# Optimization experiments

Measured on AMD Instinct MI355X. Metric: run time of the kernel, lower is better.

The kernel has to match this reference:

```python
import jax, jax.numpy as jnp
import numpy as np

B, D_IN, U, E = 8192, 1024, 1024, 16

def setup_inputs() -> dict:
    key = jax.random.key(0)
    k1, k2, k3, k4 = jax.random.split(key, 4)
    inputs = jax.random.normal(k1, (B, D_IN), dtype=jnp.float32)
    # type_prob: probability over entity types per example, [B, E, 1]
    tp = jax.random.uniform(k2, (B, E, 1), dtype=jnp.float32)
    type_prob = tp / jnp.sum(tp, axis=1, keepdims=True)
    # Stacked per-entity Dense params: W [E, D_IN, U], b [E, U]
    scale = 1.0 / np.sqrt(D_IN)
    W = jax.random.normal(k3, (E, D_IN, U), dtype=jnp.float32) * scale
    b = jax.random.normal(k4, (E, U), dtype=jnp.float32) * 0.01
    return {"inputs": inputs, "type_prob": type_prob, "W": W, "b": b}

def reference(inputs, type_prob, W, b):
    # Per-entity Dense, batched as one einsum: [B, E, U]
    logits = jnp.einsum('bd,edu->beu', inputs, W) + b
    probs = jax.nn.softmax(logits, axis=-1)  # softmax over wp_units, per entity
    # transpose to [B, U, E], matmul with type_prob [B, E, 1], reduce_sum last axis
    # == weighted combine over entities: [B, U]
    result = jnp.einsum('beu,be->bu', probs, type_prob[..., 0])
    return result
```

## Files before the change

### kernel.cpp

```cpp
#include <hip/hip_runtime.h>
#include <hip/hip_bf16.h>
#include <hip/hip_fp16.h>
#include <stdint.h>

typedef _Float16 f16;
typedef _Float16 f16x4 __attribute__((ext_vector_type(4)));
typedef _Float16 f16x8 __attribute__((ext_vector_type(8)));
typedef float f32x4 __attribute__((ext_vector_type(4)));

#define NB 8192
#define ND 1024
#define NU 1024
#define NE 16

__global__ __launch_bounds__(256) void k_prep(const float* __restrict__ W,
                                              f16* __restrict__ WT,
                                              const float* __restrict__ X,
                                              f16* __restrict__ Xh) {
  const int bid = blockIdx.x;
  const int t = threadIdx.x;
  if (bid < 4096) {
    __shared__ f16 tile[64][68];
    const int u0 = (bid & 15) * 64;
    const int d0 = ((bid >> 4) & 15) * 64;
    const int e = bid >> 8;
    const int r = t >> 4;
    const int c = (t & 15) << 2;
    const float* src = W + (size_t)e * ND * NU;
    f16* dst = WT + (size_t)e * NU * ND;
#pragma unroll
    for (int i = 0; i < 4; ++i) {
      const int rr = r + i * 16;
      const float4 v = *(const float4*)(src + (size_t)(d0 + rr) * NU + (u0 + c));
      tile[rr][c + 0] = (f16)v.x;
      tile[rr][c + 1] = (f16)v.y;
      tile[rr][c + 2] = (f16)v.z;
      tile[rr][c + 3] = (f16)v.w;
    }
    __syncthreads();
#pragma unroll
    for (int i = 0; i < 4; ++i) {
      const int rr = r + i * 16;
      f16x4 h;
      h[0] = tile[c + 0][rr];
      h[1] = tile[c + 1][rr];
      h[2] = tile[c + 2][rr];
      h[3] = tile[c + 3][rr];
      *(f16x4*)(dst + (size_t)(u0 + rr) * ND + (d0 + c)) = h;
    }
  } else {
    const size_t i = ((size_t)(bid - 4096) * 256 + t) * 8;
    const float4 v0 = *(const float4*)(X + i);
    const float4 v1 = *(const float4*)(X + i + 4);
    f16x8 h;
    h[0] = (f16)v0.x; h[1] = (f16)v0.y; h[2] = (f16)v0.z; h[3] = (f16)v0.w;
    h[4] = (f16)v1.x; h[5] = (f16)v1.y; h[6] = (f16)v1.z; h[7] = (f16)v1.w;
    *(f16x8*)(Xh + i) = h;
  }
}


typedef __attribute__((address_space(3))) void lds_void_t;
typedef __attribute__((address_space(1))) const void gbl_void_t;

__device__ __forceinline__ void gload16(const void* g, void* l) {
  __builtin_amdgcn_global_load_lds((gbl_void_t*)g, (lds_void_t*)l, 16, 0, 0);
}

#define WAIT_VM6() do { asm volatile("s_waitcnt vmcnt(6)" ::: "memory"); \
                        __builtin_amdgcn_sched_barrier(0); } while (0)
#define WAIT_VM0() do { asm volatile("s_waitcnt vmcnt(0)" ::: "memory"); \
                        __builtin_amdgcn_sched_barrier(0); } while (0)
#define WAIT_LGKM0() do { asm volatile("s_waitcnt lgkmcnt(0)" ::: "memory"); \
                          __builtin_amdgcn_sched_barrier(0); } while (0)
#define BARR() do { asm volatile("" ::: "memory"); __builtin_amdgcn_s_barrier(); \
                    asm volatile("" ::: "memory"); } while (0)

#define STAGEHP(srcp, op_b, h, kt, buf)                                         \
  {                                                                             \
    _Pragma("unroll") for (int i_ = 0; i_ < 2; ++i_) {                          \
      const unsigned s_ = i_ * 512 + t;                                         \
      const unsigned row_ = (h) * 128 + (s_ >> 3);                              \
      const unsigned sch_ = (s_ & 7) ^ (row_ & 7);                              \
      const unsigned lb_ = (unsigned)(buf) * 65536 + (op_b) * 32768 +           \
                           (h) * 16384 + (i_ * 512 + (t & ~63u)) * 16;          \
      gload16((srcp) + (size_t)row_ * 2048 + (size_t)(kt) * 128 + sch_ * 16,    \
              smem + lb_);                                                      \
    }                                                                           \
  }

#define LDA(mb0, buf)                                                           \
  _Pragma("unroll") for (int j_ = 0; j_ < 4; ++j_)                              \
    _Pragma("unroll") for (int ks_ = 0; ks_ < 2; ++ks_)                         \
      a[j_][ks_] = *(const f16x8*)(smem + (unsigned)(buf) * 65536 +             \
                     wr * 16384 + (((mb0) + j_) * 16 + ln) * 128 +              \
                     (((unsigned)(ks_ * 4 + g)) ^ (ln & 7u)) * 16);

#define LDB(buf)                                                                \
  _Pragma("unroll") for (int n_ = 0; n_ < 4; ++n_)                              \
    _Pragma("unroll") for (int ks_ = 0; ks_ < 2; ++ks_)                         \
      b[n_][ks_] = *(const f16x8*)(smem + (unsigned)(buf) * 65536 + 32768 +     \
                     (wc >> 1) * 16384 + ((wc & 1) * 64 + n_ * 16 + ln) * 128 + \
                     (((unsigned)(ks_ * 4 + g)) ^ (ln & 7u)) * 16);

#define QUAD(mb0, n0)                                                           \
  _Pragma("unroll") for (int j_ = 0; j_ < 4; ++j_)                              \
    _Pragma("unroll") for (int n_ = 0; n_ < 2; ++n_)                            \
      _Pragma("unroll") for (int ks_ = 0; ks_ < 2; ++ks_)                       \
        acc[(mb0) + j_][(n0) + n_] = __builtin_amdgcn_mfma_f32_16x16x32_f16(    \
            a[j_][ks_], b[(n0) + n_][ks_], acc[(mb0) + j_][(n0) + n_], 0, 0, 0);

__global__ __launch_bounds__(512, 2) void k_gemm_exp(const f16* __restrict__ Xc,
                                                     const f16* __restrict__ WT,
                                                     const float* __restrict__ BIAS,
                                                     f16* __restrict__ P,
                                                     float* __restrict__ S4,
                                                     int TPB, int CR) {
  __shared__ alignas(16) unsigned char smem[131072 + 4096];
  float* red = (float*)(smem + 131072);

  const int t = threadIdx.x;
  const int w = t >> 6;
  const int l = t & 63;
  const int g = l >> 4;
  const int ln = l & 15;
  const int wr = w >> 2;
  const int wc = w & 3;

  const int bid = blockIdx.x;
  const int xcd = bid & 7;
  const int i = bid >> 3;
  const int ntl = i >> 2;
  const int q = i & 3;
  const int nt = xcd * 8 + ntl;
  const int mt0 = q * TPB;

  const char* Xc0 = (const char*)Xc;
  const char* Bg = (const char*)WT + (size_t)nt * 256 * 2048;

  f32x4 acc[8][4];
#pragma unroll
  for (int mb = 0; mb < 8; ++mb)
#pragma unroll
    for (int nb = 0; nb < 4; ++nb) acc[mb][nb] = (f32x4){0.f, 0.f, 0.f, 0.f};

  f16x8 a[4][2], b[4][2];

  float bv[4];
  const float* bp = BIAS + ((size_t)(nt >> 2) << 10) + (nt & 3) * 256 + wc * 64 + ln;
#pragma unroll
  for (int nb = 0; nb < 4; ++nb) bv[nb] = bp[nb * 16];

  {
    const char* Ag0 = Xc0 + (size_t)mt0 * 256 * 2048;
    STAGEHP(Ag0, 0, 0, 0, 0); STAGEHP(Ag0, 0, 1, 0, 0);
    STAGEHP(Bg, 1, 0, 0, 0);  STAGEHP(Bg, 1, 1, 0, 0);
    STAGEHP(Bg, 1, 0, 1, 1);  STAGEHP(Bg, 1, 1, 1, 1);
    STAGEHP(Ag0, 0, 0, 1, 1);
    WAIT_VM6();
    BARR();
  }

#pragma unroll 1
  for (int ti = 0; ti < TPB; ++ti) {
    const bool last = (ti == TPB - 1);
    const char* AgC = Xc0 + (size_t)(mt0 + ti) * 256 * 2048;
    const char* AgN = Xc0 + (size_t)(mt0 + ti + (last ? 0 : 1)) * 256 * 2048;

#pragma unroll 1
    for (int k = 0; k < 16; ++k) {
      const int cur = k & 1, nxt = cur ^ 1;
      const bool sk15 = last && (k == 15);
      const bool sk14 = last && (k >= 14);
      if (sk15) { WAIT_VM0(); BARR(); }
      LDA(0, cur);
      LDB(cur);
      if (!sk15) {
        const char* s1 = (k == 15) ? AgN : AgC;
        STAGEHP(s1, 0, 1, (k + 1) & 15, nxt);
      }
      BARR();
      __builtin_amdgcn_s_setprio(1);
      QUAD(0, 0);
      __builtin_amdgcn_s_setprio(0);
      BARR();
      if (!sk14) STAGEHP(Bg, 1, 0, (k + 2) & 15, cur);
      BARR();
      __builtin_amdgcn_s_setprio(1);
      QUAD(0, 2);
      __builtin_amdgcn_s_setprio(0);
      BARR();
      LDA(4, cur);
      if (!sk14) STAGEHP(Bg, 1, 1, (k + 2) & 15, cur);
      BARR();
      __builtin_amdgcn_s_setprio(1);
      QUAD(4, 2);
      __builtin_amdgcn_s_setprio(0);
      BARR();
      if (!sk14) {
        const char* s4 = (k >= 14) ? AgN : AgC;
        STAGEHP(s4, 0, 0, (k + 2) & 15, cur);
      }
      BARR();
      __builtin_amdgcn_s_setprio(1);
      QUAD(4, 0);
      __builtin_amdgcn_s_setprio(0);
      if (!sk15) WAIT_VM6();
      BARR();
    }

    {
      const int mt = mt0 + ti;
      f16* Prow =
          P + (size_t)(mt * 256 + wr * 128) * 16384 + (size_t)nt * 256 + wc * 64 + ln;
#pragma unroll
      for (int mb = 0; mb < 8; ++mb) {
        float rs[4] = {0.f, 0.f, 0.f, 0.f};
#pragma unroll
        for (int nb = 0; nb < 4; ++nb) {
#pragma unroll
          for (int r = 0; r < 4; ++r) {
            const float p = __expf(acc[mb][nb][r] + bv[nb]);
            rs[r] += p;
            Prow[(size_t)(mb * 16 + g * 4 + r) * 16384 + nb * 16] = (f16)p;
            acc[mb][nb][r] = 0.f;
          }
        }
#pragma unroll
        for (int r = 0; r < 4; ++r) {
          float v = rs[r];
          v += __shfl_xor(v, 1);
          v += __shfl_xor(v, 2);
          v += __shfl_xor(v, 4);
          v += __shfl_xor(v, 8);
          if (ln == 0) red[(wr * 128 + mb * 16 + g * 4 + r) * 4 + wc] = v;
        }
      }
      WAIT_LGKM0();
      BARR();
      if (t < 256) {
        const float s =
            (red[t * 4 + 0] + red[t * 4 + 1]) + (red[t * 4 + 2] + red[t * 4 + 3]);
        S4[(size_t)nt * CR + mt * 256 + t] = s;
      }
      BARR();
    }
  }
}

__global__ __launch_bounds__(512) void k_combine(const f16* __restrict__ P,
                                                 const float* __restrict__ TP,
                                                 const float* __restrict__ S4,
                                                 float* __restrict__ OUT,
                                                 int RB, int CR) {
  __shared__ float c_s[4][16];
  const int t = threadIdx.x;
  const int blk = blockIdx.x;
  if (t < 64) {
    const int rr = t >> 4, e = t & 15;
    const int bl = blk * 4 + rr;
    float S = 0.f;
#pragma unroll
    for (int q = 0; q < 4; ++q) S += S4[(size_t)(e * 4 + q) * CR + bl];
    c_s[rr][e] = TP[(size_t)(RB + bl) * NE + e] / S;
  }
  __syncthreads();
  const int rl = t >> 7;
  const int bl = blk * 4 + rl;
  const int u0 = (t & 127) * 8;
  float acm[8] = {0.f, 0.f, 0.f, 0.f, 0.f, 0.f, 0.f, 0.f};
  const f16* Pb = P + (size_t)bl * 16384 + u0;
#pragma unroll
  for (int e = 0; e < NE; ++e) {
    const float c = c_s[rl][e];
    const f16x8 pv = *(const f16x8*)(Pb + e * 1024);
#pragma unroll
    for (int jj = 0; jj < 8; ++jj) acm[jj] += c * (float)pv[jj];
  }
  float* op = OUT + (size_t)(RB + bl) * NU + u0;
  *(float4*)(op) = (float4){acm[0], acm[1], acm[2], acm[3]};
  *(float4*)(op + 4) = (float4){acm[4], acm[5], acm[6], acm[7]};
}

#define BM 64
#define BUH 512
#define NRT 128
#define WT_BYTES ((size_t)NE * NU * ND * 2)
#define SUMS_FLOATS ((size_t)NE * NRT * 2 * 64)
#define FLG_INTS ((size_t)NE * NRT * 2)

#define LOADB(F, soff)                                   \
  {                                                      \
    const char* p_ = wtc + (soff) + vbase;               \
    F[0] = *(const f16x8*)(p_);                          \
    F[1] = *(const f16x8*)(p_ + 1 * 16 * ND * 2);        \
    F[2] = *(const f16x8*)(p_ + 2 * 16 * ND * 2);        \
    F[3] = *(const f16x8*)(p_ + 3 * 16 * ND * 2);        \
  }

#define MFMA_HALF(F, kbyte)                                                         \
  {                                                                                 \
    const f16x8 a0 = *(const f16x8*)(A_s + (ln + 0) * 2064 + g * 16 + (kbyte));     \
    const f16x8 a1 = *(const f16x8*)(A_s + (ln + 16) * 2064 + g * 16 + (kbyte));    \
    const f16x8 a2 = *(const f16x8*)(A_s + (ln + 32) * 2064 + g * 16 + (kbyte));    \
    const f16x8 a3 = *(const f16x8*)(A_s + (ln + 48) * 2064 + g * 16 + (kbyte));    \
    _Pragma("unroll") for (int n_ = 0; n_ < 4; ++n_) {                              \
      acc[0][n_] = __builtin_amdgcn_mfma_f32_16x16x32_f16(a0, F[n_], acc[0][n_], 0, 0, 0); \
      acc[1][n_] = __builtin_amdgcn_mfma_f32_16x16x32_f16(a1, F[n_], acc[1][n_], 0, 0, 0); \
      acc[2][n_] = __builtin_amdgcn_mfma_f32_16x16x32_f16(a2, F[n_], acc[2][n_], 0, 0, 0); \
      acc[3][n_] = __builtin_amdgcn_mfma_f32_16x16x32_f16(a3, F[n_], acc[3][n_], 0, 0, 0); \
    }                                                                               \
  }

__device__ __forceinline__ size_t wt_soff(int L) {
  L = (L > 511) ? 511 : L;
  return (size_t)(L >> 5) * ((size_t)NU * ND * 2) + (size_t)(L & 31) * 64;
}

__global__ __launch_bounds__(512, 2) void k_proj(const float* __restrict__ X,
                                                 const float* __restrict__ TP,
                                                 const f16* __restrict__ WT,
                                                 const float* __restrict__ BIAS,
                                                 float* __restrict__ OUT,
                                                 float* __restrict__ SUMS,
                                                 int* __restrict__ FLG) {
  __shared__ alignas(16) unsigned char lds[132096 + 4096 + 2048 + 256];
  unsigned char* A_s = lds;
  float* tp_s = (float*)(lds + 132096);
  float* reds = (float*)(lds + 132096 + 4096);
  float* sums_s = (float*)(lds + 132096 + 4096 + 2048);

  const int t = threadIdx.x;
  const int w = t >> 6;
  const int l = t & 63;
  const int g = l >> 4;
  const int ln = l & 15;
  const int bid = blockIdx.x;
  const int rt = bid >> 1;
  const int uh = bid & 1;
  const int b0 = rt * BM;
  const int c0 = uh * BUH;

#pragma unroll
  for (int i = 0; i < 32; ++i) {
    const int idx = (i * 512 + t) << 2;
    const int row = idx >> 10;
    const int col = idx & 1023;
    const float4 v = *(const float4*)(X + (size_t)(b0 + row) * ND + col);
    f16x4 h;
    h[0] = (f16)v.x; h[1] = (f16)v.y; h[2] = (f16)v.z; h[3] = (f16)v.w;
    *(f16x4*)(A_s + row * 2064 + (col << 1)) = h;
  }
  tp_s[t] = TP[(size_t)(b0 + (t >> 4)) * NE + (t & 15)];
  tp_s[512 + t] = TP[(size_t)(b0 + 32 + (t >> 4)) * NE + (t & 15)];
  __syncthreads();

  f32x4 out_acc[4][4];
#pragma unroll
  for (int m = 0; m < 4; ++m)
#pragma unroll
    for (int n = 0; n < 4; ++n) out_acc[m][n] = (f32x4){0.f, 0.f, 0.f, 0.f};

  const char* wtc = (const char*)WT;
  const unsigned vbase = ((unsigned)(c0 + w * 64 + ln) * ND + g * 8) * 2;

  f16x8 F0[4], F1[4], F2[4], F3[4];
  LOADB(F0, wt_soff(0));
  LOADB(F1, wt_soff(1));
  LOADB(F2, wt_soff(2));

  for (int e = 0; e < NE; ++e) {
    f32x4 acc[4][4];
#pragma unroll
    for (int m = 0; m < 4; ++m)
#pragma unroll
      for (int n = 0; n < 4; ++n) acc[m][n] = (f32x4){0.f, 0.f, 0.f, 0.f};

    const int Le = e * 32;
#pragma unroll 1
    for (int gi = 0; gi < 7; ++gi) {
      const int L = Le + gi * 4;
      const int kb = gi * 4 * 64;
      LOADB(F3, wt_soff(L + 3));
      MFMA_HALF(F0, kb + 0);
      LOADB(F0, wt_soff(L + 4));
      MFMA_HALF(F1, kb + 64);
      LOADB(F1, wt_soff(L + 5));
      MFMA_HALF(F2, kb + 128);
      LOADB(F2, wt_soff(L + 6));
      MFMA_HALF(F3, kb + 192);
    }
    LOADB(F3, wt_soff(Le + 31));
    MFMA_HALF(F0, 28 * 64);
    LOADB(F0, wt_soff(Le + 32));
    MFMA_HALF(F1, 29 * 64);
    LOADB(F1, wt_soff(Le + 33));
    MFMA_HALF(F2, 30 * 64);
    LOADB(F2, wt_soff(Le + 34));
    MFMA_HALF(F3, 31 * 64);

    const float* bp = BIAS + (size_t)e * NU + c0 + w * 64 + ln;
    float bv[4];
#pragma unroll
    for (int n = 0; n < 4; ++n) bv[n] = bp[n * 16];

    float rs[4][4];
#pragma unroll
    for (int m = 0; m < 4; ++m)
#pragma unroll
      for (int r = 0; r < 4; ++r) rs[m][r] = 0.f;
#pragma unroll
    for (int m = 0; m < 4; ++m)
#pragma unroll
      for (int n = 0; n < 4; ++n)
#pragma unroll
        for (int r = 0; r < 4; ++r) {
          const float p = __expf(acc[m][n][r] + bv[n]);
          acc[m][n][r] = p;
          rs[m][r] += p;
        }
#pragma unroll
    for (int m = 0; m < 4; ++m)
#pragma unroll
      for (int r = 0; r < 4; ++r) {
        float v = rs[m][r];
        v += __shfl_xor(v, 1, 64);
        v += __shfl_xor(v, 2, 64);
        v += __shfl_xor(v, 4, 64);
        v += __shfl_xor(v, 8, 64);
        rs[m][r] = v;
      }
    if (ln == 0) {
#pragma unroll
      for (int m = 0; m < 4; ++m)
#pragma unroll
        for (int r = 0; r < 4; ++r) reds[(m * 16 + g * 4 + r) * 8 + w] = rs[m][r];
    }
    __syncthreads();

    const int pairbase = (e * NRT + rt) * 2;
    float myS = 0.f;
    if (t < 64) {
      const float* rp = reds + t * 8;
      myS = ((rp[0] + rp[1]) + (rp[2] + rp[3])) + ((rp[4] + rp[5]) + (rp[6] + rp[7]));
      __hip_atomic_store(&SUMS[(size_t)(pairbase + uh) * 64 + t], myS,
                         __ATOMIC_RELAXED, __HIP_MEMORY_SCOPE_AGENT);
    }
    __syncthreads();
    if (t == 0) {
      __threadfence();
      __hip_atomic_store(&FLG[pairbase + uh], 1, __ATOMIC_RELEASE, __HIP_MEMORY_SCOPE_AGENT);
      int spin = 0;
      while (__hip_atomic_load(&FLG[pairbase + (uh ^ 1)], __ATOMIC_ACQUIRE,
                               __HIP_MEMORY_SCOPE_AGENT) == 0 &&
             spin < 400000) {
        __builtin_amdgcn_s_sleep(2);
        ++spin;
      }
    }
    __syncthreads();
    if (t < 64) {
      const float ps = __hip_atomic_load(&SUMS[(size_t)(pairbase + (uh ^ 1)) * 64 + t],
                                         __ATOMIC_RELAXED, __HIP_MEMORY_SCOPE_AGENT);
      sums_s[t] = myS + ps;
    }
    __syncthreads();

#pragma unroll
    for (int m = 0; m < 4; ++m)
#pragma unroll
      for (int r = 0; r < 4; ++r) {
        const int row = m * 16 + g * 4 + r;
        const float scale = tp_s[row * 16 + e] * __builtin_amdgcn_rcpf(sums_s[row]);
#pragma unroll
        for (int n = 0; n < 4; ++n) out_acc[m][n][r] += scale * acc[m][n][r];
      }
  }

#pragma unroll
  for (int m = 0; m < 4; ++m)
#pragma unroll
    for (int r = 0; r < 4; ++r) {
      float* op = OUT + (size_t)(b0 + m * 16 + g * 4 + r) * NU + c0 + w * 64 + ln;
#pragma unroll
      for (int n = 0; n < 4; ++n) op[n * 16] = out_acc[m][n][r];
    }
}

extern "C" void kernel_launch(void* const* d_in, const int* in_sizes, int n_in,
                              void* d_out, int out_size, void* d_ws, size_t ws_size,
                              hipStream_t stream) {
  const float* X = (const float*)d_in[0];
  const float* TP = (const float*)d_in[1];
  const float* W = (const float*)d_in[2];
  const float* BIAS = (const float*)d_in[3];
  float* OUT = (float*)d_out;

  const size_t XH_BYTES = (size_t)NB * ND * 2;
  const size_t FIXED = WT_BYTES + XH_BYTES;

  int CR = 0;
  for (int cr = NB; cr >= 1024; cr >>= 1) {
    const size_t need = FIXED + (size_t)cr * 16384 * 2 + (size_t)cr * 64 * 4;
    if (ws_size >= need) { CR = cr; break; }
  }

  if (CR > 0) {
    f16* WT = (f16*)d_ws;
    f16* Xh = (f16*)((char*)d_ws + WT_BYTES);
    float* S4 = (float*)((char*)d_ws + FIXED);
    f16* P = (f16*)((char*)d_ws + FIXED + (size_t)CR * 64 * 4);

    k_prep<<<dim3(8192), dim3(256), 0, stream>>>(W, WT, X, Xh);

    const int MT = CR / 256;
    const int TPB = MT / 4;
    const int nch = NB / CR;
    for (int ch = 0; ch < nch; ++ch) {
      const int RB = ch * CR;
      k_gemm_exp<<<dim3(256), dim3(512), 0, stream>>>(
          (const f16*)((const char*)Xh + (size_t)RB * ND * 2), WT, BIAS, P, S4, TPB, CR);
      k_combine<<<dim3(CR / 4), dim3(512), 0, stream>>>(P, TP, S4, OUT, RB, CR);
    }
  } else {
    f16* WT = (f16*)d_ws;
    float* SUMS = (float*)((char*)d_ws + WT_BYTES);
    int* FLG = (int*)((char*)d_ws + WT_BYTES + SUMS_FLOATS * 4);

    hipMemsetAsync(FLG, 0, FLG_INTS * sizeof(int), stream);
    k_prep<<<dim3(4096), dim3(256), 0, stream>>>(W, WT, X, nullptr);
    k_proj<<<dim3(256), dim3(512), 0, stream>>>(X, TP, WT, BIAS, OUT, SUMS, FLG);
  }
}
```

Measured before the change: 384.4 us.

## Load B operand directly from global into registers, halve LDS staging

The weight (B) tiles are no longer staged through LDS. Each wave loads its B fragments straight from global memory into registers, issued one k-step ahead. Only the A tiles are double-buffered in LDS, which halves LDS use from 128KB to 64KB, and the nested tile/k loops are flattened into one loop with fewer barriers. The aim is to cut LDS traffic and barrier overhead, at the risk of exposed global-load latency and redundant B reads across waves that share columns.

After: 461.8 us. 20.1% more time.

```diff
diff --git a/kernel.cpp b/kernel.cpp
--- a/kernel.cpp
+++ b/kernel.cpp
@@ -67,24 +67,22 @@
   __builtin_amdgcn_global_load_lds((gbl_void_t*)g, (lds_void_t*)l, 16, 0, 0);
 }
 
-#define WAIT_VM6() do { asm volatile("s_waitcnt vmcnt(6)" ::: "memory"); \
-                        __builtin_amdgcn_sched_barrier(0); } while (0)
-#define WAIT_VM0() do { asm volatile("s_waitcnt vmcnt(0)" ::: "memory"); \
+#define WAIT_VM8() do { asm volatile("s_waitcnt vmcnt(8)" ::: "memory"); \
                         __builtin_amdgcn_sched_barrier(0); } while (0)
 #define WAIT_LGKM0() do { asm volatile("s_waitcnt lgkmcnt(0)" ::: "memory"); \
                           __builtin_amdgcn_sched_barrier(0); } while (0)
 #define BARR() do { asm volatile("" ::: "memory"); __builtin_amdgcn_s_barrier(); \
                     asm volatile("" ::: "memory"); } while (0)
 
-#define STAGEHP(srcp, op_b, h, kt, buf)                                         \
+#define STAGEA(srcp, h, kl, buf)                                                \
   {                                                                             \
     _Pragma("unroll") for (int i_ = 0; i_ < 2; ++i_) {                          \
       const unsigned s_ = i_ * 512 + t;                                         \
       const unsigned row_ = (h) * 128 + (s_ >> 3);                              \
       const unsigned sch_ = (s_ & 7) ^ (row_ & 7);                              \
-      const unsigned lb_ = (unsigned)(buf) * 65536 + (op_b) * 32768 +           \
-                           (h) * 16384 + (i_ * 512 + (t & ~63u)) * 16;          \
-      gload16((srcp) + (size_t)row_ * 2048 + (size_t)(kt) * 128 + sch_ * 16,    \
+      const unsigned lb_ = (unsigned)(buf) * 32768 + (h) * 16384 +              \
+                           (i_ * 512 + (t & ~63u)) * 16;                        \
+      gload16((srcp) + (size_t)row_ * 2048 + (size_t)(kl) * 128 + sch_ * 16,    \
               smem + lb_);                                                      \
     }                                                                           \
   }
@@ -92,16 +90,15 @@
 #define LDA(mb0, buf)                                                           \
   _Pragma("unroll") for (int j_ = 0; j_ < 4; ++j_)                              \
     _Pragma("unroll") for (int ks_ = 0; ks_ < 2; ++ks_)                         \
-      a[j_][ks_] = *(const f16x8*)(smem + (unsigned)(buf) * 65536 +             \
-                     wr * 16384 + (((mb0) + j_) * 16 + ln) * 128 +              \
+      a[j_][ks_] = *(const f16x8*)(smem + (unsigned)(buf) * 32768 +             \
+                     (wr * 128 + ((mb0) + j_) * 16 + ln) * 128 +                \
                      (((unsigned)(ks_ * 4 + g)) ^ (ln & 7u)) * 16);
 
-#define LDB(buf)                                                                \
-  _Pragma("unroll") for (int n_ = 0; n_ < 4; ++n_)                              \
+#define BLOAD2(n0, kl)                                                          \
+  _Pragma("unroll") for (int n_ = (n0); n_ < (n0) + 2; ++n_)                    \
     _Pragma("unroll") for (int ks_ = 0; ks_ < 2; ++ks_)                         \
-      b[n_][ks_] = *(const f16x8*)(smem + (unsigned)(buf) * 65536 + 32768 +     \
-                     (wc >> 1) * 16384 + ((wc & 1) * 64 + n_ * 16 + ln) * 128 + \
-                     (((unsigned)(ks_ * 4 + g)) ^ (ln & 7u)) * 16);
+      b[n_][ks_] = *(const f16x8*)(Bg + (size_t)(wc * 64 + n_ * 16 + ln) * 2048 \
+                     + (size_t)(kl) * 128 + (unsigned)(ks_ * 4 + g) * 16);
 
 #define QUAD(mb0, n0)                                                           \
   _Pragma("unroll") for (int j_ = 0; j_ < 4; ++j_)                              \
@@ -116,8 +113,8 @@
                                                      f16* __restrict__ P,
                                                      float* __restrict__ S4,
                                                      int TPB, int CR) {
-  __shared__ alignas(16) unsigned char smem[131072 + 4096];
-  float* red = (float*)(smem + 131072);
+  __shared__ alignas(16) unsigned char smem[65536 + 4096];
+  float* red = (float*)(smem + 65536);
 
   const int t = threadIdx.x;
   const int w = t >> 6;
@@ -151,65 +148,53 @@
 #pragma unroll
   for (int nb = 0; nb < 4; ++nb) bv[nb] = bp[nb * 16];
 
+  const int TOT = TPB * 16;
+
   {
     const char* Ag0 = Xc0 + (size_t)mt0 * 256 * 2048;
-    STAGEHP(Ag0, 0, 0, 0, 0); STAGEHP(Ag0, 0, 1, 0, 0);
-    STAGEHP(Bg, 1, 0, 0, 0);  STAGEHP(Bg, 1, 1, 0, 0);
-    STAGEHP(Bg, 1, 0, 1, 1);  STAGEHP(Bg, 1, 1, 1, 1);
-    STAGEHP(Ag0, 0, 0, 1, 1);
-    WAIT_VM6();
+    STAGEA(Ag0, 0, 0, 0);
+    STAGEA(Ag0, 1, 0, 0);
+    __builtin_amdgcn_sched_barrier(0);
+    BLOAD2(0, 0);
+    BLOAD2(2, 0);
+    WAIT_VM8();
     BARR();
   }
 
 #pragma unroll 1
-  for (int ti = 0; ti < TPB; ++ti) {
-    const bool last = (ti == TPB - 1);
-    const char* AgC = Xc0 + (size_t)(mt0 + ti) * 256 * 2048;
-    const char* AgN = Xc0 + (size_t)(mt0 + ti + (last ? 0 : 1)) * 256 * 2048;
-
-#pragma unroll 1
-    for (int k = 0; k < 16; ++k) {
-      const int cur = k & 1, nxt = cur ^ 1;
-      const bool sk15 = last && (k == 15);
-      const bool sk14 = last && (k >= 14);
-      if (sk15) { WAIT_VM0(); BARR(); }
-      LDA(0, cur);
-      LDB(cur);
-      if (!sk15) {
-        const char* s1 = (k == 15) ? AgN : AgC;
-        STAGEHP(s1, 0, 1, (k + 1) & 15, nxt);
-      }
-      BARR();
-      __builtin_amdgcn_s_setprio(1);
-      QUAD(0, 0);
-      __builtin_amdgcn_s_setprio(0);
-      BARR();
-      if (!sk14) STAGEHP(Bg, 1, 0, (k + 2) & 15, cur);
-      BARR();
-      __builtin_amdgcn_s_setprio(1);
-      QUAD(0, 2);
-      __builtin_amdgcn_s_setprio(0);
-      BARR();
-      LDA(4, cur);
-      if (!sk14) STAGEHP(Bg, 1, 1, (k + 2) & 15, cur);
-      BARR();
-      __builtin_amdgcn_s_setprio(1);
-      QUAD(4, 2);
-      __builtin_amdgcn_s_setprio(0);
-      BARR();
-      if (!sk14) {
-        const char* s4 = (k >= 14) ? AgN : AgC;
-        STAGEHP(s4, 0, 0, (k + 2) & 15, cur);
-      }
-      BARR();
-      __builtin_amdgcn_s_setprio(1);
-      QUAD(4, 0);
-      __builtin_amdgcn_s_setprio(0);
-      if (!sk15) WAIT_VM6();
-      BARR();
-    }
-
-    {
+  for (int kt = 0; kt < TOT; ++kt) {
+    const int cur = kt & 1, nxt = cur ^ 1;
+    const int ti = kt >> 4;
+    const bool lastk = (kt == TOT - 1);
+    const int kt1 = lastk ? kt : kt + 1;
+    const int t1 = kt1 >> 4, kl1 = kt1 & 15;
+    const char* Ag1 = Xc0 + (size_t)(mt0 + t1) * 256 * 2048;
+
+    LDA(0, cur);
+    if (!lastk) {
+      STAGEA(Ag1, 0, kl1, nxt);
+      STAGEA(Ag1, 1, kl1, nxt);
+    }
+    __builtin_amdgcn_sched_barrier(0);
+    __builtin_amdgcn_s_setprio(1);
+    QUAD(0, 0);
+    QUAD(0, 2);
+    __builtin_amdgcn_s_setprio(0);
+    LDA(4, cur);
+    __builtin_amdgcn_s_setprio(1);
+    QUAD(4, 0);
+    __builtin_amdgcn_s_setprio(0);
+    if (!lastk) BLOAD2(0, kl1);
+    __builtin_amdgcn_s_setprio(1);
+    QUAD(4, 2);
+    __builtin_amdgcn_s_setprio(0);
+    if (!lastk) {
+      BLOAD2(2, kl1);
+      WAIT_VM8();
+    }
+    BARR();
+
+    if ((kt & 15) == 15) {
       const int mt = mt0 + ti;
       f16* Prow =
           P + (size_t)(mt * 256 + wr * 128) * 16384 + (size_t)nt * 256 + wc * 64 + ln;
```
